# Kernel tuning notes

Hardware: AMD Instinct MI355X
Metric: run time of the kernel (lower is better)

Reference implementation:

```python
import jax, jax.numpy as jnp
import numpy as np

N, IN_DIM, INTER, HID, OUT, G = 8192, 512, 512, 1024, 512, 16
EPS = 1e-5


def setup_inputs() -> dict:
    key = jax.random.key(0)
    ks = jax.random.split(key, 16)
    s = 0.02
    return {
        "h": jax.random.normal(ks[0], (N, IN_DIM), jnp.float32),
        "D": jax.random.uniform(ks[1], (N, N), jnp.float32),
        "h_prime": jax.random.normal(ks[2], (N, OUT), jnp.float32),
        "Qw": jax.random.normal(ks[3], (IN_DIM, INTER), jnp.float32) * s,
        "Qb": jnp.zeros((INTER,), jnp.float32),
        "Kw": jax.random.normal(ks[4], (IN_DIM, INTER), jnp.float32) * s,
        "Kb": jnp.zeros((INTER,), jnp.float32),
        "Vw": jax.random.normal(ks[5], (IN_DIM, INTER), jnp.float32) * s,
        "Vb": jnp.zeros((INTER,), jnp.float32),
        "Rw": jax.random.normal(ks[6], (INTER, HID), jnp.float32) * s,
        "Rb": jnp.zeros((HID,), jnp.float32),
        "Cw": jax.random.normal(ks[7], (OUT, HID), jnp.float32) * s,
        "Cb": jnp.zeros((HID,), jnp.float32),
        "Pw": jax.random.normal(ks[8], (2 * HID, OUT), jnp.float32) * s,
        "Pb": jnp.zeros((OUT,), jnp.float32),
        "prelu_a": jnp.full((OUT,), 0.25, jnp.float32),  # PReLU default init
        "gn_w": jnp.ones((OUT,), jnp.float32),
        "gn_b": jnp.zeros((OUT,), jnp.float32),
    }


def reference(h, D, h_prime, Qw, Qb, Kw, Kb, Vw, Vb, Rw, Rb, Cw, Cb, Pw, Pb, prelu_a, gn_w, gn_b):
    Q = h @ Qw + Qb                      # (N, inter)
    K = h @ Kw + Kb
    V = h @ Vw + Vb
    scores = D * (Q @ K.T)               # (N, N), decayed retention scores
    h_ret = scores @ V                   # (N, inter)
    h_ret = jax.nn.gelu(h_ret @ Rw + Rb, approximate=False)   # (N, hid)
    h_cat = h_prime @ Cw + Cb            # (N, hid)
    combined = jnp.concatenate([h_ret, h_cat], axis=-1)       # (N, 2*hid)
    x = combined @ Pw + Pb               # (N, out)
    x = jnp.where(x >= 0, x, prelu_a * x)                      # PReLU per-channel
    # GroupNorm over channel groups per row: (N, G, out/G)
    xg = x.reshape(N, G, OUT // G)
    mu = xg.mean(axis=-1, keepdims=True)
    var = xg.var(axis=-1, keepdims=True)
    xn = ((xg - mu) * jax.lax.rsqrt(var + EPS)).reshape(N, OUT)
    return xn * gn_w + gn_b
```

## Files before the change

kernel.cpp:

```cpp
#include <hip/hip_runtime.h>
#include <math.h>

typedef __attribute__((ext_vector_type(8))) short bf16x8;
typedef __attribute__((ext_vector_type(4))) float f32x4;
typedef __attribute__((ext_vector_type(8))) unsigned short u16x8;

#define DEVFN __device__ __forceinline__
#define AS1 __attribute__((address_space(1)))
#define AS3 __attribute__((address_space(3)))

DEVFN unsigned short f2bf(float f) {
    unsigned int u = __float_as_uint(f);
    u += 0x7fffu + ((u >> 16) & 1u);
    return (unsigned short)(u >> 16);
}
DEVFN float bf2f(unsigned short u) {
    unsigned int x = ((unsigned int)u) << 16;
    return __uint_as_float(x);
}

__global__ void cast2_kernel(const float* __restrict__ a, const float* __restrict__ b,
                             unsigned short* __restrict__ oa, unsigned short* __restrict__ ob,
                             int n8) {
    const float* in = blockIdx.y ? b : a;
    unsigned short* out = blockIdx.y ? ob : oa;
    int i = blockIdx.x * blockDim.x + threadIdx.x;
    if (i >= n8) return;
    const float4* p = reinterpret_cast<const float4*>(in) + (size_t)i * 2;
    float4 x = p[0], y = p[1];
    u16x8 o;
    o[0] = f2bf(x.x); o[1] = f2bf(x.y); o[2] = f2bf(x.z); o[3] = f2bf(x.w);
    o[4] = f2bf(y.x); o[5] = f2bf(y.y); o[6] = f2bf(y.z); o[7] = f2bf(y.w);
    reinterpret_cast<u16x8*>(out)[i] = o;
}

__global__ void sum4b_kernel(const unsigned short* __restrict__ p, size_t stride,
                             unsigned short* __restrict__ out, int n8) {
    int i = blockIdx.x * blockDim.x + threadIdx.x;
    if (i >= n8) return;
    u16x8 a = reinterpret_cast<const u16x8*>(p)[i];
    u16x8 b = reinterpret_cast<const u16x8*>(p + stride)[i];
    u16x8 c = reinterpret_cast<const u16x8*>(p + 2 * stride)[i];
    u16x8 d = reinterpret_cast<const u16x8*>(p + 3 * stride)[i];
    u16x8 o;
#pragma unroll
    for (int j = 0; j < 8; ++j)
        o[j] = f2bf(bf2f(a[j]) + bf2f(b[j]) + bf2f(c[j]) + bf2f(d[j]));
    reinterpret_cast<u16x8*>(out)[i] = o;
}

__global__ void concat_bias_kernel(const float* __restrict__ a,
                                   const float* __restrict__ b,
                                   const float* __restrict__ c,
                                   float* __restrict__ o) {
    int i = blockIdx.x * blockDim.x + threadIdx.x;
    if (i >= 1536) return;
    o[i] = i < 512 ? a[i] : (i < 1024 ? b[i - 512] : c[i - 1024]);
}

struct TD { const float* in; unsigned short* out; int ldin, ldout, nbx, nby; };
struct TD6 { TD d[6]; };

__global__ void multi_transpose_kernel(TD6 t6) {
    TD d = t6.d[blockIdx.z];
    if ((int)blockIdx.x >= d.nbx || (int)blockIdx.y >= d.nby) return;
    __shared__ unsigned short tile[32][34];
    int c0 = blockIdx.x * 32, r0 = blockIdx.y * 32;
    int tx = threadIdx.x, ty = threadIdx.y;
#pragma unroll
    for (int i = 0; i < 32; i += 8)
        tile[ty + i][tx] = f2bf(d.in[(size_t)(r0 + ty + i) * d.ldin + c0 + tx]);
    __syncthreads();
#pragma unroll
    for (int i = 0; i < 32; i += 8)
        d.out[(size_t)(c0 + ty + i) * d.ldout + r0 + tx] = tile[tx][ty + i];
}

__global__ void transpose_bf16_kernel(const unsigned short* __restrict__ in, int ldin,
                                      unsigned short* __restrict__ out, int ldout) {
    __shared__ unsigned short tile[32][34];
    int c0 = blockIdx.x * 32, r0 = blockIdx.y * 32;
    int tx = threadIdx.x, ty = threadIdx.y;
#pragma unroll
    for (int i = 0; i < 32; i += 8)
        tile[ty + i][tx] = in[(size_t)(r0 + ty + i) * ldin + c0 + tx];
    __syncthreads();
#pragma unroll
    for (int i = 0; i < 32; i += 8)
        out[(size_t)(c0 + ty + i) * ldout + r0 + tx] = tile[tx][ty + i];
}

enum { EP_BF16_BIAS = 0, EP_DMUL_LDS = 1, EP_PART16 = 2, EP_PRELU_GN = 4, EP_DUAL = 5 };

template <int MODE>
__global__ __launch_bounds__(256, 2) void gemm_bt_kernel(
    const unsigned short* __restrict__ A, int lda,
    const unsigned short* __restrict__ B, int ldb,
    void* __restrict__ Cv, int ldc, int K,
    const float* __restrict__ bias,
    const float* __restrict__ Dmul, int ldd, size_t zstride,
    const float* __restrict__ PA, const float* __restrict__ GW,
    const float* __restrict__ GB,
    const unsigned short* __restrict__ A2,
    const unsigned short* __restrict__ B2,
    const float* __restrict__ bias2) {
    __shared__ alignas(16) unsigned char SMEM[65536];
    unsigned short (*As)[8192] = (unsigned short(*)[8192])SMEM;
    unsigned short (*Bs)[8192] = (unsigned short(*)[8192])(SMEM + 32768);

    unsigned bx, by, zi = 0;
    if (MODE == EP_PART16) {
        unsigned gx = gridDim.x;
        unsigned L = (blockIdx.z * gridDim.y + blockIdx.y) * gx + blockIdx.x;
        unsigned xcd = L & 7u, slot = L >> 3;
        zi = xcd >> 1;
        unsigned t = slot * 2 + (xcd & 1u);
        bx = t & (gx - 1);
        by = t / gx;
    } else {
        unsigned nwg = gridDim.x * gridDim.y;
        unsigned bid = blockIdx.y * gridDim.x + blockIdx.x;
        unsigned cpx = nwg >> 3;
        bid = (bid & 7u) * cpx + (bid >> 3);
        bx = bid % gridDim.x;
        by = bid / gridDim.x;
    }
    size_t m0 = (size_t)by * 128;
    size_t nB = (size_t)bx * 128;
    size_t ncol0 = nB;

    const unsigned short* Ause = A;
    const unsigned short* Buse = B;
    const float* bias_use = bias;
    bool apply_gelu = false;
    if (MODE == EP_DUAL) {
        unsigned half = gridDim.x >> 1;
        if (bx >= half) {
            nB = (size_t)(bx - half) * 128;
            ncol0 = 1024 + nB;
            Ause = A2; Buse = B2; bias_use = bias2;
        } else {
            apply_gelu = true;
        }
    }

    int tid = threadIdx.x;
    int lane = tid & 63, w = tid >> 6;
    int wr = w >> 1, wc = w & 1;
    int cif = lane & 15;
    int rif = (lane >> 4) << 2;

    f32x4 acc[4][4];
#pragma unroll
    for (int i = 0; i < 4; ++i)
#pragma unroll
        for (int j = 0; j < 4; ++j)
#pragma unroll
            for (int r = 0; r < 4; ++r) acc[i][j][r] = 0.f;

    const unsigned short* Ablk = Ause + m0 * lda + (size_t)zi * K;
    const unsigned short* Bblk = Buse + nB * ldb + (size_t)zi * K;
    int srccol = ((lane & 7) ^ (lane >> 3)) * 8;
    int srow = w * 32 + (lane >> 3);
    int nkt = K >> 6;

    auto stage = [&](int buf, int kt) {
        int k0 = kt << 6;
        unsigned short* la = &As[buf][w * 2048];
        unsigned short* lb = &Bs[buf][w * 2048];
#pragma unroll
        for (int i = 0; i < 4; ++i) {
            __builtin_amdgcn_global_load_lds(
                (const AS1 void*)(Ablk + (size_t)(srow + i * 8) * lda + k0 + srccol),
                (AS3 void*)(la + i * 512), 16, 0, 0);
            __builtin_amdgcn_global_load_lds(
                (const AS1 void*)(Bblk + (size_t)(srow + i * 8) * ldb + k0 + srccol),
                (AS3 void*)(lb + i * 512), 16, 0, 0);
        }
    };

    stage(0, 0);
    __syncthreads();

    for (int kt = 0; kt < nkt; ++kt) {
        int cur = kt & 1;
        if (kt + 1 < nkt) stage(cur ^ 1, kt + 1);

        const bf16x8* Ap = reinterpret_cast<const bf16x8*>(As[cur]);
        const bf16x8* Bp = reinterpret_cast<const bf16x8*>(Bs[cur]);
#pragma unroll
        for (int kk = 0; kk < 2; ++kk) {
            bf16x8 af[4], bfr[4];
#pragma unroll
            for (int mi = 0; mi < 4; ++mi) {
                int row = wr * 64 + mi * 16 + (lane & 15);
                int slot = ((kk << 2) + (lane >> 4)) ^ (row & 7);
                af[mi] = Ap[row * 8 + slot];
            }
#pragma unroll
            for (int ni = 0; ni < 4; ++ni) {
                int row = wc * 64 + ni * 16 + (lane & 15);
                int slot = ((kk << 2) + (lane >> 4)) ^ (row & 7);
                bfr[ni] = Bp[row * 8 + slot];
            }
#pragma unroll
            for (int mi = 0; mi < 4; ++mi)
#pragma unroll
                for (int ni = 0; ni < 4; ++ni)
                    acc[mi][ni] = __builtin_amdgcn_mfma_f32_16x16x32_bf16(
                        af[mi], bfr[ni], acc[mi][ni], 0, 0, 0);
        }
        __syncthreads();
    }

    if (MODE == EP_DMUL_LDS) {
        float4* Dl4 = (float4*)SMEM;
        int f4c = tid & 31;
        int r0 = tid >> 5;
        float4 dv[16];
#pragma unroll
        for (int j = 0; j < 16; ++j)
            dv[j] = ((const float4*)(Dmul + (m0 + r0 + j * 8) * (size_t)ldd + ncol0))[f4c];
#pragma unroll
        for (int j = 0; j < 16; ++j)
            Dl4[(r0 + j * 8) * 32 + f4c] = dv[j];
        __syncthreads();
        const float* Dl = (const float*)SMEM;
        unsigned short* Cb16 = (unsigned short*)Cv;
#pragma unroll
        for (int mi = 0; mi < 4; ++mi) {
#pragma unroll
            for (int ni = 0; ni < 4; ++ni) {
                int lcol = wc * 64 + ni * 16 + cif;
                size_t gcol = ncol0 + lcol;
#pragma unroll
                for (int r = 0; r < 4; ++r) {
                    int lrow = wr * 64 + mi * 16 + rif + r;
                    float v = acc[mi][ni][r] * Dl[lrow * 128 + lcol];
                    Cb16[(m0 + lrow) * (size_t)ldc + gcol] = f2bf(v);
                }
            }
        }
        return;
    }

    if (MODE == EP_PART16) {
        unsigned short* Cp = (unsigned short*)Cv + zi * zstride;
#pragma unroll
        for (int mi = 0; mi < 4; ++mi)
#pragma unroll
            for (int ni = 0; ni < 4; ++ni) {
                size_t gcol = ncol0 + wc * 64 + ni * 16 + cif;
#pragma unroll
                for (int r = 0; r < 4; ++r) {
                    size_t grow = m0 + wr * 64 + mi * 16 + rif + r;
                    Cp[grow * (size_t)ldc + gcol] = f2bf(acc[mi][ni][r]);
                }
            }
        return;
    }

    if (MODE == EP_PRELU_GN) {
        float* Cf = (float*)Cv;
        float pbv[4], pav[4], gwv[4], gbv[4];
        size_t gcolv[4];
#pragma unroll
        for (int ni = 0; ni < 4; ++ni) {
            gcolv[ni] = ncol0 + wc * 64 + ni * 16 + cif;
            pbv[ni] = bias[gcolv[ni]];
            pav[ni] = PA[gcolv[ni]];
            gwv[ni] = GW[gcolv[ni]];
            gbv[ni] = GB[gcolv[ni]];
        }
#pragma unroll
        for (int mi = 0; mi < 4; ++mi) {
#pragma unroll
            for (int ni = 0; ni < 4; ++ni)
#pragma unroll
                for (int r = 0; r < 4; ++r) {
                    float v = acc[mi][ni][r] + pbv[ni];
                    acc[mi][ni][r] = v >= 0.f ? v : pav[ni] * v;
                }
#pragma unroll
            for (int p = 0; p < 2; ++p) {
                float s[4], ss[4];
#pragma unroll
                for (int r = 0; r < 4; ++r) {
                    float a0 = acc[mi][2 * p][r], a1 = acc[mi][2 * p + 1][r];
                    s[r] = a0 + a1;
                    ss[r] = a0 * a0 + a1 * a1;
                }
#pragma unroll
                for (int msk = 1; msk < 16; msk <<= 1)
#pragma unroll
                    for (int r = 0; r < 4; ++r) {
                        s[r] += __shfl_xor(s[r], msk);
                        ss[r] += __shfl_xor(ss[r], msk);
                    }
#pragma unroll
                for (int r = 0; r < 4; ++r) {
                    float mu = s[r] * (1.f / 32.f);
                    float inv = rsqrtf(ss[r] * (1.f / 32.f) - mu * mu + 1e-5f);
                    size_t grow = m0 + wr * 64 + mi * 16 + rif + r;
#pragma unroll
                    for (int q = 0; q < 2; ++q) {
                        int ni = 2 * p + q;
                        Cf[grow * (size_t)ldc + gcolv[ni]] =
                            (acc[mi][ni][r] - mu) * inv * gwv[ni] + gbv[ni];
                    }
                }
            }
        }
        return;
    }

#pragma unroll
    for (int mi = 0; mi < 4; ++mi) {
#pragma unroll
        for (int ni = 0; ni < 4; ++ni) {
            size_t gcol = ncol0 + wc * 64 + ni * 16 + cif;
            size_t bcol = nB + wc * 64 + ni * 16 + cif;
            float bval = bias_use ? bias_use[bcol] : 0.f;
#pragma unroll
            for (int r = 0; r < 4; ++r) {
                size_t grow = m0 + wr * 64 + mi * 16 + rif + r;
                float val = acc[mi][ni][r] + bval;
                if (MODE == EP_DUAL && apply_gelu)
                    val = 0.5f * val * (1.f + erff(val * 0.70710678118654752f));
                ((unsigned short*)Cv)[grow * (size_t)ldc + gcol] = f2bf(val);
            }
        }
    }
}

extern "C" void kernel_launch(void* const* d_in, const int* in_sizes, int n_in,
                              void* d_out, int out_size, void* d_ws, size_t ws_size,
                              hipStream_t stream) {
    constexpr int Nn = 8192, IND = 512, INTER = 512, HID = 1024, OUTD = 512;
    const float* h   = (const float*)d_in[0];
    const float* Dm  = (const float*)d_in[1];
    const float* hp  = (const float*)d_in[2];
    const float* Qw  = (const float*)d_in[3];
    const float* Qb  = (const float*)d_in[4];
    const float* Kw  = (const float*)d_in[5];
    const float* Kb  = (const float*)d_in[6];
    const float* Vw  = (const float*)d_in[7];
    const float* Vb  = (const float*)d_in[8];
    const float* Rw  = (const float*)d_in[9];
    const float* Rb  = (const float*)d_in[10];
    const float* Cw  = (const float*)d_in[11];
    const float* Cb  = (const float*)d_in[12];
    const float* Pw  = (const float*)d_in[13];
    const float* Pb  = (const float*)d_in[14];
    const float* pa  = (const float*)d_in[15];
    const float* gwt = (const float*)d_in[16];
    const float* gbt = (const float*)d_in[17];
    (void)in_sizes; (void)n_in; (void)out_size; (void)ws_size;

    char* ws = (char*)d_ws;
    size_t cur = 0;
    auto alloc = [&](size_t bytes) -> void* {
        void* p = ws + cur;
        cur += (bytes + 255) & ~(size_t)255;
        return p;
    };
    unsigned short* h_bf   = (unsigned short*)alloc((size_t)Nn * IND * 2);
    unsigned short* hp_bf  = (unsigned short*)alloc((size_t)Nn * OUTD * 2);
    unsigned short* QKVwT  = (unsigned short*)alloc((size_t)3 * INTER * IND * 2);
    float*          qkvb   = (float*)alloc((size_t)3 * INTER * 4);
    unsigned short* RwT    = (unsigned short*)alloc((size_t)INTER * HID * 2);
    unsigned short* CwT    = (unsigned short*)alloc((size_t)OUTD * HID * 2);
    unsigned short* PwT    = (unsigned short*)alloc((size_t)2 * HID * OUTD * 2);
    unsigned short* QKVm   = (unsigned short*)alloc((size_t)Nn * 3 * INTER * 2);
    unsigned short* VTm    = (unsigned short*)alloc((size_t)Nn * INTER * 2);
    unsigned short* Sm     = (unsigned short*)alloc((size_t)Nn * Nn * 2);
    unsigned short* hret_p = (unsigned short*)alloc((size_t)4 * Nn * INTER * 2);
    unsigned short* hretbf = (unsigned short*)alloc((size_t)Nn * INTER * 2);
    unsigned short* comb   = Sm;

    unsigned short* Qm = QKVm;
    unsigned short* Km = QKVm + INTER;
    unsigned short* Vm = QKVm + 2 * INTER;
    const int ldqkv = 3 * INTER;

    dim3 tb(32, 8);
    int n8 = Nn * IND / 8;
    cast2_kernel<<<dim3(n8 / 256, 2), 256, 0, stream>>>(h, hp, h_bf, hp_bf, n8);

    TD6 t6;
    t6.d[0] = {Qw, QKVwT,                          INTER, IND,     16, 16};
    t6.d[1] = {Kw, QKVwT + (size_t)INTER * IND,    INTER, IND,     16, 16};
    t6.d[2] = {Vw, QKVwT + (size_t)2 * INTER * IND,INTER, IND,     16, 16};
    t6.d[3] = {Rw, RwT,                            HID,   INTER,   32, 16};
    t6.d[4] = {Cw, CwT,                            HID,   OUTD,    32, 16};
    t6.d[5] = {Pw, PwT,                            OUTD,  2 * HID, 16, 64};
    multi_transpose_kernel<<<dim3(32, 64, 6), tb, 0, stream>>>(t6);
    concat_bias_kernel<<<6, 256, 0, stream>>>(Qb, Kb, Vb, qkvb);

    gemm_bt_kernel<EP_BF16_BIAS><<<dim3(3 * INTER / 128, Nn / 128), 256, 0, stream>>>(
        h_bf, IND, QKVwT, IND, QKVm, ldqkv, IND, qkvb, nullptr, 0, 0,
        nullptr, nullptr, nullptr, nullptr, nullptr, nullptr);
    transpose_bf16_kernel<<<dim3(INTER / 32, Nn / 32), tb, 0, stream>>>(Vm, ldqkv, VTm, Nn);

    gemm_bt_kernel<EP_DMUL_LDS><<<dim3(Nn / 128, Nn / 128), 256, 0, stream>>>(
        Qm, ldqkv, Km, ldqkv, Sm, Nn, INTER, nullptr, Dm, Nn, 0,
        nullptr, nullptr, nullptr, nullptr, nullptr, nullptr);

    gemm_bt_kernel<EP_PART16><<<dim3(OUTD / 128, Nn / 128, 4), 256, 0, stream>>>(
        Sm, Nn, VTm, Nn, hret_p, INTER, Nn / 4, nullptr, nullptr, 0, (size_t)Nn * INTER,
        nullptr, nullptr, nullptr, nullptr, nullptr, nullptr);
    sum4b_kernel<<<(Nn * INTER / 8) / 256, 256, 0, stream>>>(
        hret_p, (size_t)Nn * INTER, hretbf, Nn * INTER / 8);

    gemm_bt_kernel<EP_DUAL><<<dim3(2 * HID / 128, Nn / 128), 256, 0, stream>>>(
        hretbf, INTER, RwT, INTER, comb, 2 * HID, INTER, Rb, nullptr, 0, 0,
        nullptr, nullptr, nullptr, hp_bf, CwT, Cb);

    gemm_bt_kernel<EP_PRELU_GN><<<dim3(OUTD / 128, Nn / 128), 256, 0, stream>>>(
        comb, 2 * HID, PwT, 2 * HID, d_out, OUTD, 2 * HID, Pb, nullptr, 0, 0,
        pa, gwt, gbt, nullptr, nullptr, nullptr);
}
```

Before: 368.5 us.

## Halve GEMM K-tile to 32, shrink LDS to 32KB, raise occupancy to 4

The shared GEMM kernel now stages 32-wide K tiles in a 32KB double buffer instead of 64-wide tiles in 64KB, with a new swizzled LDS layout. The launch bound rises from 2 to 4 blocks per SIMD group so more workgroups can be resident and hide latency. The D-multiply epilogue no longer stages D through LDS and instead reads it straight from global memory with a strided per-lane pattern. The cost is twice as many K iterations and barriers, possible register spilling under the tighter launch bound, and less coalesced D reads.

New measurement: 417.7 us. +13.3%, slower.

```diff
diff --git a/kernel.cpp b/kernel.cpp
--- a/kernel.cpp
+++ b/kernel.cpp
@@ -90,10 +90,10 @@
         out[(size_t)(c0 + ty + i) * ldout + r0 + tx] = tile[tx][ty + i];
 }
 
-enum { EP_BF16_BIAS = 0, EP_DMUL_LDS = 1, EP_PART16 = 2, EP_PRELU_GN = 4, EP_DUAL = 5 };
+enum { EP_BF16_BIAS = 0, EP_DMUL = 1, EP_PART16 = 2, EP_PRELU_GN = 4, EP_DUAL = 5 };
 
 template <int MODE>
-__global__ __launch_bounds__(256, 2) void gemm_bt_kernel(
+__global__ __launch_bounds__(256, 4) void gemm_bt_kernel(
     const unsigned short* __restrict__ A, int lda,
     const unsigned short* __restrict__ B, int ldb,
     void* __restrict__ Cv, int ldc, int K,
@@ -104,9 +104,7 @@
     const unsigned short* __restrict__ A2,
     const unsigned short* __restrict__ B2,
     const float* __restrict__ bias2) {
-    __shared__ alignas(16) unsigned char SMEM[65536];
-    unsigned short (*As)[8192] = (unsigned short(*)[8192])SMEM;
-    unsigned short (*Bs)[8192] = (unsigned short(*)[8192])(SMEM + 32768);
+    __shared__ alignas(16) unsigned short SM16[16384];
 
     unsigned bx, by, zi = 0;
     if (MODE == EP_PART16) {
@@ -147,6 +145,7 @@
     int tid = threadIdx.x;
     int lane = tid & 63, w = tid >> 6;
     int wr = w >> 1, wc = w & 1;
+    int l15 = lane & 15;
     int cif = lane & 15;
     int rif = (lane >> 4) << 2;
 
@@ -160,22 +159,29 @@
 
     const unsigned short* Ablk = Ause + m0 * lda + (size_t)zi * K;
     const unsigned short* Bblk = Buse + nB * ldb + (size_t)zi * K;
-    int srccol = ((lane & 7) ^ (lane >> 3)) * 8;
-    int srow = w * 32 + (lane >> 3);
-    int nkt = K >> 6;
+    int nkt = K >> 5;
+
+    int slog = (lane & 7) ^ ((lane >> 3) & 7);
+    int srowoff = (slog >> 2) * 64;
+    int scoloff = (slog & 3) * 8;
+    int aslot = ((wr << 2) + (lane >> 4)) ^ (lane & 7);
+    int bslot = ((wc << 2) + (lane >> 4)) ^ (lane & 7);
 
     auto stage = [&](int buf, int kt) {
-        int k0 = kt << 6;
-        unsigned short* la = &As[buf][w * 2048];
-        unsigned short* lb = &Bs[buf][w * 2048];
-#pragma unroll
-        for (int i = 0; i < 4; ++i) {
+        int k0 = kt << 5;
+#pragma unroll
+        for (int j = 0; j < 2; ++j) {
+            int crb = j * 32 + w * 8;
+            int cr = crb + (lane >> 3);
+            int srow = cr + srowoff;
+            unsigned short* la = SM16 + buf * 8192 + crb * 64 + lane * 8;
+            unsigned short* lb = la + 4096;
             __builtin_amdgcn_global_load_lds(
-                (const AS1 void*)(Ablk + (size_t)(srow + i * 8) * lda + k0 + srccol),
-                (AS3 void*)(la + i * 512), 16, 0, 0);
+                (const AS1 void*)(Ablk + (size_t)srow * lda + k0 + scoloff),
+                (AS3 void*)la, 16, 0, 0);
             __builtin_amdgcn_global_load_lds(
-                (const AS1 void*)(Bblk + (size_t)(srow + i * 8) * ldb + k0 + srccol),
-                (AS3 void*)(lb + i * 512), 16, 0, 0);
+                (const AS1 void*)(Bblk + (size_t)srow * ldb + k0 + scoloff),
+                (AS3 void*)lb, 16, 0, 0);
         }
     };
 
@@ -186,58 +192,36 @@
         int cur = kt & 1;
         if (kt + 1 < nkt) stage(cur ^ 1, kt + 1);
 
-        const bf16x8* Ap = reinterpret_cast<const bf16x8*>(As[cur]);
-        const bf16x8* Bp = reinterpret_cast<const bf16x8*>(Bs[cur]);
-#pragma unroll
-        for (int kk = 0; kk < 2; ++kk) {
-            bf16x8 af[4], bfr[4];
-#pragma unroll
-            for (int mi = 0; mi < 4; ++mi) {
-                int row = wr * 64 + mi * 16 + (lane & 15);
-                int slot = ((kk << 2) + (lane >> 4)) ^ (row & 7);
-                af[mi] = Ap[row * 8 + slot];
-            }
+        const bf16x8* Ap = reinterpret_cast<const bf16x8*>(SM16 + cur * 8192);
+        const bf16x8* Bp = reinterpret_cast<const bf16x8*>(SM16 + cur * 8192 + 4096);
+        bf16x8 af[4], bfr[4];
+#pragma unroll
+        for (int mi = 0; mi < 4; ++mi)
+            af[mi] = Ap[(mi * 16 + l15) * 8 + aslot];
+#pragma unroll
+        for (int ni = 0; ni < 4; ++ni)
+            bfr[ni] = Bp[(ni * 16 + l15) * 8 + bslot];
+#pragma unroll
+        for (int mi = 0; mi < 4; ++mi)
+#pragma unroll
+            for (int ni = 0; ni < 4; ++ni)
+                acc[mi][ni] = __builtin_amdgcn_mfma_f32_16x16x32_bf16(
+                    af[mi], bfr[ni], acc[mi][ni], 0, 0, 0);
+        __syncthreads();
+    }
+
+    if (MODE == EP_DMUL) {
+        unsigned short* Cb16 = (unsigned short*)Cv;
+#pragma unroll
+        for (int mi = 0; mi < 4; ++mi) {
 #pragma unroll
             for (int ni = 0; ni < 4; ++ni) {
-                int row = wc * 64 + ni * 16 + (lane & 15);
-                int slot = ((kk << 2) + (lane >> 4)) ^ (row & 7);
-                bfr[ni] = Bp[row * 8 + slot];
-            }
-#pragma unroll
-            for (int mi = 0; mi < 4; ++mi)
-#pragma unroll
-                for (int ni = 0; ni < 4; ++ni)
-                    acc[mi][ni] = __builtin_amdgcn_mfma_f32_16x16x32_bf16(
-                        af[mi], bfr[ni], acc[mi][ni], 0, 0, 0);
-        }
-        __syncthreads();
-    }
-
-    if (MODE == EP_DMUL_LDS) {
-        float4* Dl4 = (float4*)SMEM;
-        int f4c = tid & 31;
-        int r0 = tid >> 5;
-        float4 dv[16];
-#pragma unroll
-        for (int j = 0; j < 16; ++j)
-            dv[j] = ((const float4*)(Dmul + (m0 + r0 + j * 8) * (size_t)ldd + ncol0))[f4c];
-#pragma unroll
-        for (int j = 0; j < 16; ++j)
-            Dl4[(r0 + j * 8) * 32 + f4c] = dv[j];
-        __syncthreads();
-        const float* Dl = (const float*)SMEM;
-        unsigned short* Cb16 = (unsigned short*)Cv;
-#pragma unroll
-        for (int mi = 0; mi < 4; ++mi) {
-#pragma unroll
-            for (int ni = 0; ni < 4; ++ni) {
-                int lcol = wc * 64 + ni * 16 + cif;
-                size_t gcol = ncol0 + lcol;
+                size_t gcol = ncol0 + wc * 64 + ni * 16 + cif;
 #pragma unroll
                 for (int r = 0; r < 4; ++r) {
-                    int lrow = wr * 64 + mi * 16 + rif + r;
-                    float v = acc[mi][ni][r] * Dl[lrow * 128 + lcol];
-                    Cb16[(m0 + lrow) * (size_t)ldc + gcol] = f2bf(v);
+                    size_t grow = m0 + wr * 64 + mi * 16 + rif + r;
+                    float v = acc[mi][ni][r] * Dmul[grow * (size_t)ldd + gcol];
+                    Cb16[grow * (size_t)ldc + gcol] = f2bf(v);
                 }
             }
         }
@@ -402,7 +386,7 @@
         nullptr, nullptr, nullptr, nullptr, nullptr, nullptr);
     transpose_bf16_kernel<<<dim3(INTER / 32, Nn / 32), tb, 0, stream>>>(Vm, ldqkv, VTm, Nn);
 
-    gemm_bt_kernel<EP_DMUL_LDS><<<dim3(Nn / 128, Nn / 128), 256, 0, stream>>>(
+    gemm_bt_kernel<EP_DMUL><<<dim3(Nn / 128, Nn / 128), 256, 0, stream>>>(
         Qm, ldqkv, Km, ldqkv, Sm, Nn, INTER, nullptr, Dm, Nn, 0,
         nullptr, nullptr, nullptr, nullptr, nullptr, nullptr);
 
```

## Chunk score matrix along key dimension to keep S tile resident in cache

Applied to the files above, without the earlier changes.

Instead of materializing the full 8192x8192 bf16 score matrix, the retention stage is split into four key-column chunks of 2048. Each chunk's scores are computed and then consumed by a split-K partial GEMM writing two partial outputs, and the eight partials are summed at the end. The aim is to shrink the S buffer to 32 MB so it stays in the MI355X's last-level cache between producer and consumer, cutting HBM traffic. In exchange it launches more kernels, adds more partial-sum traffic, and gives each launch a smaller grid.

Result: slower. 392.1 us (+6.4%).

```diff
diff --git a/kernel.cpp b/kernel.cpp
--- a/kernel.cpp
+++ b/kernel.cpp
@@ -34,18 +34,20 @@
     reinterpret_cast<u16x8*>(out)[i] = o;
 }
 
-__global__ void sum4b_kernel(const unsigned short* __restrict__ p, size_t stride,
+__global__ void sum8b_kernel(const unsigned short* __restrict__ p, size_t stride,
                              unsigned short* __restrict__ out, int n8) {
     int i = blockIdx.x * blockDim.x + threadIdx.x;
     if (i >= n8) return;
-    u16x8 a = reinterpret_cast<const u16x8*>(p)[i];
-    u16x8 b = reinterpret_cast<const u16x8*>(p + stride)[i];
-    u16x8 c = reinterpret_cast<const u16x8*>(p + 2 * stride)[i];
-    u16x8 d = reinterpret_cast<const u16x8*>(p + 3 * stride)[i];
+    float acc[8] = {0.f, 0.f, 0.f, 0.f, 0.f, 0.f, 0.f, 0.f};
+#pragma unroll
+    for (int k = 0; k < 8; ++k) {
+        u16x8 v = reinterpret_cast<const u16x8*>(p + k * stride)[i];
+#pragma unroll
+        for (int j = 0; j < 8; ++j) acc[j] += bf2f(v[j]);
+    }
     u16x8 o;
 #pragma unroll
-    for (int j = 0; j < 8; ++j)
-        o[j] = f2bf(bf2f(a[j]) + bf2f(b[j]) + bf2f(c[j]) + bf2f(d[j]));
+    for (int j = 0; j < 8; ++j) o[j] = f2bf(acc[j]);
     reinterpret_cast<u16x8*>(out)[i] = o;
 }
 
@@ -111,11 +113,13 @@
     unsigned bx, by, zi = 0;
     if (MODE == EP_PART16) {
         unsigned gx = gridDim.x;
+        unsigned nz = gridDim.z;
+        unsigned xpz = 8u / nz;
         unsigned L = (blockIdx.z * gridDim.y + blockIdx.y) * gx + blockIdx.x;
         unsigned xcd = L & 7u, slot = L >> 3;
-        zi = xcd >> 1;
-        unsigned t = slot * 2 + (xcd & 1u);
-        bx = t & (gx - 1);
+        zi = xcd / xpz;
+        unsigned t = slot * xpz + (xcd % xpz);
+        bx = t % gx;
         by = t / gx;
     } else {
         unsigned nwg = gridDim.x * gridDim.y;
@@ -337,6 +341,7 @@
                               void* d_out, int out_size, void* d_ws, size_t ws_size,
                               hipStream_t stream) {
     constexpr int Nn = 8192, IND = 512, INTER = 512, HID = 1024, OUTD = 512;
+    constexpr int CH = 2048;
     const float* h   = (const float*)d_in[0];
     const float* Dm  = (const float*)d_in[1];
     const float* hp  = (const float*)d_in[2];
@@ -373,10 +378,10 @@
     unsigned short* PwT    = (unsigned short*)alloc((size_t)2 * HID * OUTD * 2);
     unsigned short* QKVm   = (unsigned short*)alloc((size_t)Nn * 3 * INTER * 2);
     unsigned short* VTm    = (unsigned short*)alloc((size_t)Nn * INTER * 2);
-    unsigned short* Sm     = (unsigned short*)alloc((size_t)Nn * Nn * 2);
-    unsigned short* hret_p = (unsigned short*)alloc((size_t)4 * Nn * INTER * 2);
+    unsigned short* Sm     = (unsigned short*)alloc((size_t)Nn * CH * 2);
+    unsigned short* hret_p = (unsigned short*)alloc((size_t)8 * Nn * INTER * 2);
     unsigned short* hretbf = (unsigned short*)alloc((size_t)Nn * INTER * 2);
-    unsigned short* comb   = Sm;
+    unsigned short* comb   = (unsigned short*)alloc((size_t)Nn * 2 * HID * 2);
 
     unsigned short* Qm = QKVm;
     unsigned short* Km = QKVm + INTER;
@@ -402,14 +407,18 @@
         nullptr, nullptr, nullptr, nullptr, nullptr, nullptr);
     transpose_bf16_kernel<<<dim3(INTER / 32, Nn / 32), tb, 0, stream>>>(Vm, ldqkv, VTm, Nn);
 
-    gemm_bt_kernel<EP_DMUL_LDS><<<dim3(Nn / 128, Nn / 128), 256, 0, stream>>>(
-        Qm, ldqkv, Km, ldqkv, Sm, Nn, INTER, nullptr, Dm, Nn, 0,
-        nullptr, nullptr, nullptr, nullptr, nullptr, nullptr);
-
-    gemm_bt_kernel<EP_PART16><<<dim3(OUTD / 128, Nn / 128, 4), 256, 0, stream>>>(
-        Sm, Nn, VTm, Nn, hret_p, INTER, Nn / 4, nullptr, nullptr, 0, (size_t)Nn * INTER,
-        nullptr, nullptr, nullptr, nullptr, nullptr, nullptr);
-    sum4b_kernel<<<(Nn * INTER / 8) / 256, 256, 0, stream>>>(
+    for (int c = 0; c < Nn / CH; ++c) {
+        int c0 = c * CH;
+        gemm_bt_kernel<EP_DMUL_LDS><<<dim3(CH / 128, Nn / 128), 256, 0, stream>>>(
+            Qm, ldqkv, Km + (size_t)c0 * ldqkv, ldqkv, Sm, CH, INTER,
+            nullptr, Dm + c0, Nn, 0,
+            nullptr, nullptr, nullptr, nullptr, nullptr, nullptr);
+        gemm_bt_kernel<EP_PART16><<<dim3(OUTD / 128, Nn / 128, 2), 256, 0, stream>>>(
+            Sm, CH, VTm + c0, Nn, hret_p + (size_t)2 * c * Nn * INTER, INTER, CH / 2,
+            nullptr, nullptr, 0, (size_t)Nn * INTER,
+            nullptr, nullptr, nullptr, nullptr, nullptr, nullptr);
+    }
+    sum8b_kernel<<<(Nn * INTER / 8) / 256, 256, 0, stream>>>(
         hret_p, (size_t)Nn * INTER, hretbf, Nn * INTER / 8);
 
     gemm_bt_kernel<EP_DUAL><<<dim3(2 * HID / 128, Nn / 128), 256, 0, stream>>>(
```

## Prefetch decay matrix into registers during QK^T main loop with compile-time K

Applied to the files above, without the earlier changes.

The Q·K^T scores kernel now issues per-thread global loads of its D tile during the fully unrolled K loop (K fixed at compile time), instead of loading D into LDS after the GEMM finishes. This hides the latency of reading the large fp32 D matrix behind MFMA work and drops the extra LDS round trip and barrier. It also adds an XCD-aware block remapping so neighbouring row tiles share L2. The cost is 64 extra registers per thread for D values, which may hurt occupancy or cause spills, and volatile inline asm loads can limit compiler scheduling.

Result: slower. 394.0 us (+6.9%).

```diff
diff --git a/kernel.cpp b/kernel.cpp
--- a/kernel.cpp
+++ b/kernel.cpp
@@ -90,13 +90,13 @@
         out[(size_t)(c0 + ty + i) * ldout + r0 + tx] = tile[tx][ty + i];
 }
 
-enum { EP_BF16_BIAS = 0, EP_DMUL_LDS = 1, EP_PART16 = 2, EP_PRELU_GN = 4, EP_DUAL = 5 };
-
-template <int MODE>
+enum { EP_BF16_BIAS = 0, EP_DMUL = 1, EP_PART16 = 2, EP_PRELU_GN = 4, EP_DUAL = 5 };
+
+template <int MODE, int KCT = 0>
 __global__ __launch_bounds__(256, 2) void gemm_bt_kernel(
     const unsigned short* __restrict__ A, int lda,
     const unsigned short* __restrict__ B, int ldb,
-    void* __restrict__ Cv, int ldc, int K,
+    void* __restrict__ Cv, int ldc, int Krt,
     const float* __restrict__ bias,
     const float* __restrict__ Dmul, int ldd, size_t zstride,
     const float* __restrict__ PA, const float* __restrict__ GW,
@@ -104,12 +104,18 @@
     const unsigned short* __restrict__ A2,
     const unsigned short* __restrict__ B2,
     const float* __restrict__ bias2) {
-    __shared__ alignas(16) unsigned char SMEM[65536];
-    unsigned short (*As)[8192] = (unsigned short(*)[8192])SMEM;
-    unsigned short (*Bs)[8192] = (unsigned short(*)[8192])(SMEM + 32768);
+    __shared__ alignas(16) unsigned short As[2][8192];
+    __shared__ alignas(16) unsigned short Bs[2][8192];
+
+    const int K = KCT ? KCT : Krt;
 
     unsigned bx, by, zi = 0;
-    if (MODE == EP_PART16) {
+    if (MODE == EP_DMUL) {
+        unsigned bid = blockIdx.y * gridDim.x + blockIdx.x;
+        unsigned xcd = bid & 7u, slot = bid >> 3;
+        by = xcd * 8 + (slot & 7u);
+        bx = slot >> 3;
+    } else if (MODE == EP_PART16) {
         unsigned gx = gridDim.x;
         unsigned L = (blockIdx.z * gridDim.y + blockIdx.y) * gx + blockIdx.x;
         unsigned xcd = L & 7u, slot = L >> 3;
@@ -179,65 +185,115 @@
         }
     };
 
+    float dreg[8][8];
+    size_t dcolv[4];
+    if (MODE == EP_DMUL) {
+#pragma unroll
+        for (int ni = 0; ni < 4; ++ni)
+            dcolv[ni] = ncol0 + wc * 64 + ni * 16 + cif;
+    }
+
     stage(0, 0);
     __syncthreads();
 
-    for (int kt = 0; kt < nkt; ++kt) {
-        int cur = kt & 1;
-        if (kt + 1 < nkt) stage(cur ^ 1, kt + 1);
-
-        const bf16x8* Ap = reinterpret_cast<const bf16x8*>(As[cur]);
-        const bf16x8* Bp = reinterpret_cast<const bf16x8*>(Bs[cur]);
-#pragma unroll
-        for (int kk = 0; kk < 2; ++kk) {
-            bf16x8 af[4], bfr[4];
-#pragma unroll
-            for (int mi = 0; mi < 4; ++mi) {
-                int row = wr * 64 + mi * 16 + (lane & 15);
-                int slot = ((kk << 2) + (lane >> 4)) ^ (row & 7);
-                af[mi] = Ap[row * 8 + slot];
-            }
+#pragma unroll
+    for (int kt = 0; kt < (KCT ? (KCT >> 6) : 1) * (KCT ? 1 : 0) + (KCT ? 0 : 0); ++kt) {}
+
+    if (KCT) {
+#pragma unroll
+        for (int kt = 0; kt < (KCT >> 6); ++kt) {
+            int cur = kt & 1;
+            if (kt + 1 < (KCT >> 6)) stage(cur ^ 1, kt + 1);
+
+            if (MODE == EP_DMUL) {
+                const int mi = kt >> 1, rp = kt & 1;
+#pragma unroll
+                for (int rr = 0; rr < 2; ++rr) {
+                    const float* rowp =
+                        Dmul + (m0 + wr * 64 + mi * 16 + rif + rp * 2 + rr) * (size_t)ldd;
+#pragma unroll
+                    for (int ni = 0; ni < 4; ++ni) {
+                        const float* p = rowp + dcolv[ni];
+                        asm volatile("global_load_dword %0, %1, off"
+                                     : "=v"(dreg[kt][ni * 2 + rr])
+                                     : "v"(p)
+                                     : "memory");
+                    }
+                }
+            }
+
+            const bf16x8* Ap = reinterpret_cast<const bf16x8*>(As[cur]);
+            const bf16x8* Bp = reinterpret_cast<const bf16x8*>(Bs[cur]);
+#pragma unroll
+            for (int kk = 0; kk < 2; ++kk) {
+                bf16x8 af[4], bfr[4];
+#pragma unroll
+                for (int mi = 0; mi < 4; ++mi) {
+                    int row = wr * 64 + mi * 16 + (lane & 15);
+                    int slot = ((kk << 2) + (lane >> 4)) ^ (row & 7);
+                    af[mi] = Ap[row * 8 + slot];
+                }
+#pragma unroll
+                for (int ni = 0; ni < 4; ++ni) {
+                    int row = wc * 64 + ni * 16 + (lane & 15);
+                    int slot = ((kk << 2) + (lane >> 4)) ^ (row & 7);
+                    bfr[ni] = Bp[row * 8 + slot];
+                }
+#pragma unroll
+                for (int mi = 0; mi < 4; ++mi)
+#pragma unroll
+                    for (int ni = 0; ni < 4; ++ni)
+                        acc[mi][ni] = __builtin_amdgcn_mfma_f32_16x16x32_bf16(
+                            af[mi], bfr[ni], acc[mi][ni], 0, 0, 0);
+            }
+            __syncthreads();
+        }
+    } else {
+        for (int kt = 0; kt < nkt; ++kt) {
+            int cur = kt & 1;
+            if (kt + 1 < nkt) stage(cur ^ 1, kt + 1);
+
+            const bf16x8* Ap = reinterpret_cast<const bf16x8*>(As[cur]);
+            const bf16x8* Bp = reinterpret_cast<const bf16x8*>(Bs[cur]);
+#pragma unroll
+            for (int kk = 0; kk < 2; ++kk) {
+                bf16x8 af[4], bfr[4];
+#pragma unroll
+                for (int mi = 0; mi < 4; ++mi) {
+                    int row = wr * 64 + mi * 16 + (lane & 15);
+                    int slot = ((kk << 2) + (lane >> 4)) ^ (row & 7);
+                    af[mi] = Ap[row * 8 + slot];
+                }
+#pragma unroll
+                for (int ni = 0; ni < 4; ++ni) {
+                    int row = wc * 64 + ni * 16 + (lane & 15);
+                    int slot = ((kk << 2) + (lane >> 4)) ^ (row & 7);
+                    bfr[ni] = Bp[row * 8 + slot];
+                }
+#pragma unroll
+                for (int mi = 0; mi < 4; ++mi)
+#pragma unroll
+                    for (int ni = 0; ni < 4; ++ni)
+                        acc[mi][ni] = __builtin_amdgcn_mfma_f32_16x16x32_bf16(
+                            af[mi], bfr[ni], acc[mi][ni], 0, 0, 0);
+            }
+            __syncthreads();
+        }
+    }
+
+    if (MODE == EP_DMUL) {
+        unsigned short* Cb16 = (unsigned short*)Cv;
+#pragma unroll
+        for (int mi = 0; mi < 4; ++mi) {
 #pragma unroll
             for (int ni = 0; ni < 4; ++ni) {
-                int row = wc * 64 + ni * 16 + (lane & 15);
-                int slot = ((kk << 2) + (lane >> 4)) ^ (row & 7);
-                bfr[ni] = Bp[row * 8 + slot];
-            }
-#pragma unroll
-            for (int mi = 0; mi < 4; ++mi)
-#pragma unroll
-                for (int ni = 0; ni < 4; ++ni)
-                    acc[mi][ni] = __builtin_amdgcn_mfma_f32_16x16x32_bf16(
-                        af[mi], bfr[ni], acc[mi][ni], 0, 0, 0);
-        }
-        __syncthreads();
-    }
-
-    if (MODE == EP_DMUL_LDS) {
-        float4* Dl4 = (float4*)SMEM;
-        int f4c = tid & 31;
-        int r0 = tid >> 5;
-        float4 dv[16];
-#pragma unroll
-        for (int j = 0; j < 16; ++j)
-            dv[j] = ((const float4*)(Dmul + (m0 + r0 + j * 8) * (size_t)ldd + ncol0))[f4c];
-#pragma unroll
-        for (int j = 0; j < 16; ++j)
-            Dl4[(r0 + j * 8) * 32 + f4c] = dv[j];
-        __syncthreads();
-        const float* Dl = (const float*)SMEM;
-        unsigned short* Cb16 = (unsigned short*)Cv;
-#pragma unroll
-        for (int mi = 0; mi < 4; ++mi) {
-#pragma unroll
-            for (int ni = 0; ni < 4; ++ni) {
-                int lcol = wc * 64 + ni * 16 + cif;
-                size_t gcol = ncol0 + lcol;
+                size_t gcol = ncol0 + wc * 64 + ni * 16 + cif;
 #pragma unroll
                 for (int r = 0; r < 4; ++r) {
-                    int lrow = wr * 64 + mi * 16 + rif + r;
-                    float v = acc[mi][ni][r] * Dl[lrow * 128 + lcol];
-                    Cb16[(m0 + lrow) * (size_t)ldc + gcol] = f2bf(v);
+                    size_t grow = m0 + wr * 64 + mi * 16 + rif + r;
+                    float dv = dreg[mi * 2 + (r >> 1)][ni * 2 + (r & 1)];
+                    float v = acc[mi][ni][r] * dv;
+                    Cb16[grow * (size_t)ldc + gcol] = f2bf(v);
                 }
             }
         }
@@ -402,7 +458,7 @@
         nullptr, nullptr, nullptr, nullptr, nullptr, nullptr);
     transpose_bf16_kernel<<<dim3(INTER / 32, Nn / 32), tb, 0, stream>>>(Vm, ldqkv, VTm, Nn);
 
-    gemm_bt_kernel<EP_DMUL_LDS><<<dim3(Nn / 128, Nn / 128), 256, 0, stream>>>(
+    gemm_bt_kernel<EP_DMUL, 512><<<dim3(Nn / 128, Nn / 128), 256, 0, stream>>>(
         Qm, ldqkv, Km, ldqkv, Sm, Nn, INTER, nullptr, Dm, Nn, 0,
         nullptr, nullptr, nullptr, nullptr, nullptr, nullptr);
 
```
